# Kernel tuning notes

Measured on AMD Instinct MI355X. Metric: run time of the kernel, lower is better.

The kernel has to match this reference:

```python
import jax, jax.numpy as jnp
import numpy as np

N, E, F, S, R, H = 10000, 160000, 128, 10, 8, 64
SH_OFF = [0, 1, 4, 9]
SH_DIM = [1, 3, 5, 7]
AVG_NUM_NEIGHBORS = 16.0


def setup_inputs() -> dict:
    key = jax.random.key(0)
    ks = jax.random.split(key, 16)
    species = jax.random.randint(ks[0], (N,), 0, S)
    node_attrs = jax.nn.one_hot(species, S, dtype=jnp.float32)
    node_feats = jax.random.normal(ks[1], (N, F), dtype=jnp.float32)
    edge_attrs = jax.random.normal(ks[2], (E, 16), dtype=jnp.float32)
    edge_feats = jax.random.normal(ks[3], (E, R), dtype=jnp.float32)
    edge_index = jax.random.randint(ks[4], (2, E), 0, N)
    # learned parameters
    W_skip_node = jax.random.normal(ks[5], (F, S, F), dtype=jnp.float32)
    W_up = jax.random.normal(ks[6], (F, F), dtype=jnp.float32)
    mlp_w1 = jax.random.normal(ks[7], (R, H), dtype=jnp.float32)
    mlp_w2 = jax.random.normal(ks[8], (H, H), dtype=jnp.float32)
    mlp_w3 = jax.random.normal(ks[9], (H, H), dtype=jnp.float32)
    mlp_w4 = jax.random.normal(ks[10], (H, 4 * F), dtype=jnp.float32)  # conv_tp.weight_numel = 512
    W_lin = jax.random.normal(ks[11], (4, F, F), dtype=jnp.float32)
    W_skip_msg = jax.random.normal(ks[12], (4, F, S, F), dtype=jnp.float32)
    W_out = jax.random.normal(ks[13], (F, F), dtype=jnp.float32)
    return dict(node_attrs=node_attrs, node_feats=node_feats, edge_attrs=edge_attrs,
                edge_feats=edge_feats, edge_index=edge_index, species=species,
                W_skip_node=W_skip_node, W_up=W_up, mlp_w1=mlp_w1, mlp_w2=mlp_w2,
                mlp_w3=mlp_w3, mlp_w4=mlp_w4, W_lin=W_lin, W_skip_msg=W_skip_msg,
                W_out=W_out)


def reference(node_attrs, node_feats, edge_attrs, edge_feats, edge_index, species,
              W_skip_node, W_up, mlp_w1, mlp_w2, mlp_w3, mlp_w4,
              W_lin, W_skip_msg, W_out):
    sender, receiver = edge_index[0], edge_index[1]
    num_nodes = node_feats.shape[0]
    num_edges = edge_attrs.shape[0]

    # skip_tp_node: FullyConnectedTensorProduct(128x0e, 10x0e -> 128x0e), fan_in = 128*10
    skip = jnp.einsum('nu,nv,uvw->nw', node_feats, node_attrs, W_skip_node) * (1.0 / np.sqrt(F * S))

    # linear_up: 128x0e -> 128x0e
    h = (node_feats @ W_up) * (1.0 / np.sqrt(F))

    # radial MLP (e3nn FullyConnectedNet: no bias, w/sqrt(fan_in), silu on hidden layers)
    t = edge_feats
    for W in (mlp_w1, mlp_w2, mlp_w3):
        t = jax.nn.silu((t @ W) * (1.0 / np.sqrt(W.shape[0])))
    tp_w = (t @ mlp_w4) * (1.0 / np.sqrt(H))  # [E, 512]

    # conv_tp (gather -> 0e x l -> l 'uvu' TP) fused with scatter_sum per l-block
    hs = h[sender]  # [E, 128]
    msgs = []
    for l in range(4):
        d = SH_DIM[l]
        w_l = tp_w[:, l * F:(l + 1) * F]                       # [E, 128]
        sh_l = edge_attrs[:, SH_OFF[l]:SH_OFF[l] + d]          # [E, d]
        mji = (hs * w_l)[:, :, None] * sh_l[:, None, :]        # [E, 128, d]
        m = jax.ops.segment_sum(mji.reshape(num_edges, F * d), receiver,
                                num_segments=num_nodes)
        msgs.append(m.reshape(num_nodes, F, d))

    inv_avg = 1.0 / np.sqrt(AVG_NUM_NEIGHBORS)
    # linear (per-l 128->128) / sqrt(avg_num_neighbors), then skip_tp_msg (x 10x0e attrs)
    blocks = []
    for l in range(4):
        x = jnp.einsum('num,uw->nwm', msgs[l], W_lin[l]) * (inv_avg / np.sqrt(F))
        x = jnp.einsum('num,nv,uvw->nwm', x, node_attrs, W_skip_msg[l]) * (1.0 / np.sqrt(F * S))
        blocks.append(x)

    # linear_out: target -> 128x0e keeps only the scalar (l=0) block
    message = (blocks[0][:, :, 0] @ W_out) * (1.0 / np.sqrt(F))  # [N, 128]
    return message, skip
```

## Files before the change

### kernel.cpp

```cpp
#include <hip/hip_runtime.h>
#include <math.h>

#define NFEAT 128
#define NSPEC 10

__global__ void k_histboth(const int* __restrict__ species, const int* __restrict__ edge_index,
                           int* __restrict__ counts, int* __restrict__ ehist, int N, int E) {
    int i = blockIdx.x * blockDim.x + threadIdx.x;
    if (i < N) atomicAdd(&counts[species[i]], 1);
    if (i < E) atomicAdd(&ehist[edge_index[E + i]], 1);
}

__global__ void k_build(const int* __restrict__ counts, int* __restrict__ cursor,
                        int4* __restrict__ table, int* __restrict__ nTiles) {
    __shared__ int off[NSPEC + 1], ts[NSPEC + 1], cnt[NSPEC];
    const int t = threadIdx.x;
    if (t == 0) {
        int o = 0, tt = 0;
        for (int s = 0; s < NSPEC; s++) {
            cnt[s] = counts[s];
            off[s] = o; ts[s] = tt;
            o += cnt[s]; tt += (cnt[s] + 63) >> 6;
        }
        off[NSPEC] = o; ts[NSPEC] = tt;
        nTiles[0] = tt;
    }
    __syncthreads();
    if (t < NSPEC) cursor[t] = off[t];
    int nt = ts[NSPEC];
    for (int i = t; i < nt; i += blockDim.x) {
        int s = 0;
        while (ts[s + 1] <= i) s++;
        int b = i - ts[s];
        table[i] = make_int4(s, off[s] + b * 64, min(64, cnt[s] - b * 64), 0);
    }
}

__global__ void k_scatter(const int* __restrict__ species, int* __restrict__ cursor,
                          int* __restrict__ sorted, int N) {
    int i = blockIdx.x * blockDim.x + threadIdx.x;
    if (i < N) {
        int p = atomicAdd(&cursor[species[i]], 1);
        sorted[p] = i;
    }
}

__global__ void k_escan(const int* __restrict__ ehist, int* __restrict__ ecursor, int N) {
    __shared__ int ssum[256];
    const int t = threadIdx.x;
    const int chunk = (N + 255) / 256;
    const int lo = t * chunk;
    const int hi = min(lo + chunk, N);
    int local = 0;
    for (int i = lo; i < hi; i++) local += ehist[i];
    ssum[t] = local;
    __syncthreads();
    for (int off = 1; off < 256; off <<= 1) {
        int x = (t >= off) ? ssum[t - off] : 0;
        __syncthreads();
        ssum[t] += x;
        __syncthreads();
    }
    int run = ssum[t] - local;
    for (int i = lo; i < hi; i++) {
        ecursor[i] = run;
        run += ehist[i];
    }
}

__global__ void k_egather(const int* __restrict__ edge_index, const float* __restrict__ edge_attrs,
                          const float* __restrict__ edge_feats, int* __restrict__ ecursor,
                          int* __restrict__ sendG, int* __restrict__ recvG,
                          float* __restrict__ sh0G, float* __restrict__ efG, int E) {
    int i = blockIdx.x * blockDim.x + threadIdx.x;
    if (i < E) {
        int r = edge_index[E + i];
        int p = atomicAdd(&ecursor[r], 1);
        sendG[p] = edge_index[i];
        recvG[p] = r;
        sh0G[p]  = edge_attrs[(long)i * 16];
        float4 v0 = *(const float4*)(edge_feats + (long)i * 8);
        float4 v1 = *(const float4*)(edge_feats + (long)i * 8 + 4);
        *(float4*)(efG + (long)p * 8)     = v0;
        *(float4*)(efG + (long)p * 8 + 4) = v1;
    }
}

template <int BC>
__global__ __launch_bounds__(256) void k_gemm(
    const float* __restrict__ A, int aStride,
    const float* __restrict__ B, int bStride, int bSpecStride,
    float* __restrict__ C, int cStride, int cChunkY,
    int M, float alpha,
    const int* __restrict__ sorted,
    const int4* __restrict__ table,
    const int* __restrict__ nTiles)
{
    __shared__ float At[128][64];
    __shared__ float Bs[128][BC];
    const int t = threadIdx.x;
    const int gy = blockIdx.y;

    int start, cnt, spec = 0;
    if (table) {
        if (blockIdx.x >= nTiles[0]) return;
        int4 te = table[blockIdx.x];
        spec = te.x; start = te.y; cnt = te.z;
    } else {
        start = blockIdx.x * 64;
        cnt = M - start;
        if (cnt <= 0) return;
        if (cnt > 64) cnt = 64;
    }

    {
        const float* Bp = B + (long)spec * bSpecStride + (long)gy * BC;
        constexpr int F4R = BC / 4;
        #pragma unroll
        for (int i = 0; i < (128 * F4R) / 256; i++) {
            int idx = t + 256 * i;
            int k = idx / F4R;
            int c = (idx % F4R) * 4;
            *(float4*)&Bs[k][c] = *(const float4*)(Bp + (long)k * bStride + c);
        }
    }
    {
        int r = t & 63;
        int kc = (t >> 6) * 32;
        if (r < cnt) {
            int grow = table ? sorted[start + r] : (start + r);
            const float4* src = (const float4*)(A + (long)grow * aStride + kc);
            #pragma unroll
            for (int i = 0; i < 8; i++) {
                float4 v = src[i];
                At[kc + 4*i + 0][r] = v.x;
                At[kc + 4*i + 1][r] = v.y;
                At[kc + 4*i + 2][r] = v.z;
                At[kc + 4*i + 3][r] = v.w;
            }
        } else {
            #pragma unroll
            for (int i = 0; i < 32; i++) At[kc + i][r] = 0.0f;
        }
    }
    __syncthreads();

    constexpr int CG   = BC / 4;
    constexpr int ROWS = BC / 16;
    const int c0 = (t % CG) * 4;
    const int r0 = (t / CG) * ROWS;
    float acc[ROWS][4] = {};
    #pragma unroll 8
    for (int k = 0; k < 128; k++) {
        float4 b = *(const float4*)&Bs[k][c0];
        float av[ROWS];
        #pragma unroll
        for (int i = 0; i < ROWS / 4; i++) {
            float4 a = *(const float4*)&At[k][r0 + 4 * i];
            av[4*i + 0] = a.x; av[4*i + 1] = a.y; av[4*i + 2] = a.z; av[4*i + 3] = a.w;
        }
        #pragma unroll
        for (int i = 0; i < ROWS; i++) {
            acc[i][0] += av[i] * b.x;
            acc[i][1] += av[i] * b.y;
            acc[i][2] += av[i] * b.z;
            acc[i][3] += av[i] * b.w;
        }
    }
    #pragma unroll
    for (int i = 0; i < ROWS; i++) {
        int r = r0 + i;
        if (r < cnt) {
            int grow = table ? sorted[start + r] : (start + r);
            float4 v = make_float4(acc[i][0] * alpha, acc[i][1] * alpha,
                                   acc[i][2] * alpha, acc[i][3] * alpha);
            *(float4*)&C[(long)gy * cChunkY + (long)grow * cStride + c0] = v;
        }
    }
}

__global__ __launch_bounds__(256) void k_edge(
    const int*   __restrict__ sendG,
    const int*   __restrict__ recvG,
    const float* __restrict__ sh0G,
    const float* __restrict__ efG,
    const float* __restrict__ W1,
    const float* __restrict__ W2,
    const float* __restrict__ W3,
    const float* __restrict__ W4,
    const float* __restrict__ h,
    float*       __restrict__ msgs0,
    int E)
{
    __shared__ float W1s[8][64];
    __shared__ float W2s[64][64];
    __shared__ float act[64][64];
    __shared__ float efT[8][64];
    __shared__ int   sendS[64];
    __shared__ int   recvS[64];
    __shared__ float sh0S[64];

    const int t = threadIdx.x;
    if (t < 128) ((float4*)W1s)[t] = ((const float4*)W1)[t];
    #pragma unroll
    for (int i = 0; i < 4; i++)
        ((float4*)W2s)[t + 256 * i] = ((const float4*)W2)[t + 256 * i];
    __syncthreads();

    const float s1 = 0.3535533905932738f;
    const float s2 = 0.125f;

    const int e0 = (t & 15) * 4;
    const int j0 = (t >> 4) * 4;

    int ntiles = (E + 63) >> 6;
    for (int tile = blockIdx.x; tile < ntiles; tile += gridDim.x) {
        int ebase = tile << 6;
        if (t < 64) {
            int p = ebase + t;
            if (p < E) {
                sendS[t] = sendG[p];
                recvS[t] = recvG[p];
                sh0S[t]  = sh0G[p];
            } else { sendS[t] = 0; recvS[t] = -1; sh0S[t] = 0.0f; }
        } else if (t < 128) {
            int l = t - 64;
            int p = ebase + l;
            if (p < E) {
                float4 v0 = *(const float4*)(efG + (long)p * 8);
                float4 v1 = *(const float4*)(efG + (long)p * 8 + 4);
                efT[0][l] = v0.x; efT[1][l] = v0.y; efT[2][l] = v0.z; efT[3][l] = v0.w;
                efT[4][l] = v1.x; efT[5][l] = v1.y; efT[6][l] = v1.z; efT[7][l] = v1.w;
            } else {
                #pragma unroll
                for (int k = 0; k < 8; k++) efT[k][l] = 0.0f;
            }
        }
        __syncthreads();

        {
            float acc[4][4] = {};
            #pragma unroll
            for (int k = 0; k < 8; k++) {
                float4 a = *(const float4*)&efT[k][e0];
                float4 b = *(const float4*)&W1s[k][j0];
                float av[4] = {a.x, a.y, a.z, a.w};
                float bv[4] = {b.x, b.y, b.z, b.w};
                #pragma unroll
                for (int jj = 0; jj < 4; jj++)
                    #pragma unroll
                    for (int ee = 0; ee < 4; ee++)
                        acc[jj][ee] += av[ee] * bv[jj];
            }
            #pragma unroll
            for (int jj = 0; jj < 4; jj++) {
                float4 v; float x;
                x = acc[jj][0] * s1; v.x = x / (1.0f + __expf(-x));
                x = acc[jj][1] * s1; v.y = x / (1.0f + __expf(-x));
                x = acc[jj][2] * s1; v.z = x / (1.0f + __expf(-x));
                x = acc[jj][3] * s1; v.w = x / (1.0f + __expf(-x));
                *(float4*)&act[j0 + jj][e0] = v;
            }
        }
        __syncthreads();

        {
            float acc[4][4] = {};
            #pragma unroll 4
            for (int k = 0; k < 64; k++) {
                float4 a = *(const float4*)&act[k][e0];
                float4 b = *(const float4*)&W2s[k][j0];
                float av[4] = {a.x, a.y, a.z, a.w};
                float bv[4] = {b.x, b.y, b.z, b.w};
                #pragma unroll
                for (int jj = 0; jj < 4; jj++)
                    #pragma unroll
                    for (int ee = 0; ee < 4; ee++)
                        acc[jj][ee] += av[ee] * bv[jj];
            }
            __syncthreads();
            #pragma unroll
            for (int jj = 0; jj < 4; jj++) {
                float4 v; float x;
                x = acc[jj][0] * s2; v.x = x / (1.0f + __expf(-x));
                x = acc[jj][1] * s2; v.y = x / (1.0f + __expf(-x));
                x = acc[jj][2] * s2; v.z = x / (1.0f + __expf(-x));
                x = acc[jj][3] * s2; v.w = x / (1.0f + __expf(-x));
                *(float4*)&act[j0 + jj][e0] = v;
            }
        }
        __syncthreads();

        {
            float acc[4][4] = {};
            #pragma unroll 4
            for (int k = 0; k < 64; k++) {
                float4 a = *(const float4*)&act[k][e0];
                float4 b = *(const float4*)(W3 + k * 64 + j0);
                float av[4] = {a.x, a.y, a.z, a.w};
                float bv[4] = {b.x, b.y, b.z, b.w};
                #pragma unroll
                for (int jj = 0; jj < 4; jj++)
                    #pragma unroll
                    for (int ee = 0; ee < 4; ee++)
                        acc[jj][ee] += av[ee] * bv[jj];
            }
            __syncthreads();
            #pragma unroll
            for (int jj = 0; jj < 4; jj++) {
                float4 v; float x;
                x = acc[jj][0] * s2; v.x = x / (1.0f + __expf(-x));
                x = acc[jj][1] * s2; v.y = x / (1.0f + __expf(-x));
                x = acc[jj][2] * s2; v.z = x / (1.0f + __expf(-x));
                x = acc[jj][3] * s2; v.w = x / (1.0f + __expf(-x));
                *(float4*)&act[j0 + jj][e0] = v;
            }
        }
        __syncthreads();

        {
            const int c0  = (t & 31) * 4;
            const int ew0 = (t >> 5) * 8;
            float acc[8][4] = {};
            #pragma unroll 4
            for (int k = 0; k < 64; k++) {
                float4 b  = *(const float4*)&W4[k * 512 + c0];
                float4 a0 = *(const float4*)&act[k][ew0];
                float4 a1 = *(const float4*)&act[k][ew0 + 4];
                float av[8] = {a0.x, a0.y, a0.z, a0.w, a1.x, a1.y, a1.z, a1.w};
                #pragma unroll
                for (int i = 0; i < 8; i++) {
                    acc[i][0] += av[i] * b.x;
                    acc[i][1] += av[i] * b.y;
                    acc[i][2] += av[i] * b.z;
                    acc[i][3] += av[i] * b.w;
                }
            }
            float4 sum = make_float4(0.f, 0.f, 0.f, 0.f);
            int cur = recvS[ew0];
            #pragma unroll
            for (int i = 0; i < 8; i++) {
                int el = ew0 + i;
                int rcv = recvS[el];
                float f = sh0S[el] * s2;
                int snd = sendS[el];
                float4 hv = *(const float4*)&h[(long)snd * NFEAT + c0];
                float4 v = make_float4(acc[i][0] * f * hv.x, acc[i][1] * f * hv.y,
                                       acc[i][2] * f * hv.z, acc[i][3] * f * hv.w);
                if (rcv != cur) {
                    if (cur >= 0) {
                        float* dst = msgs0 + (long)cur * NFEAT + c0;
                        atomicAdd(dst + 0, sum.x); atomicAdd(dst + 1, sum.y);
                        atomicAdd(dst + 2, sum.z); atomicAdd(dst + 3, sum.w);
                    }
                    cur = rcv; sum = v;
                } else {
                    sum.x += v.x; sum.y += v.y; sum.z += v.z; sum.w += v.w;
                }
            }
            if (cur >= 0) {
                float* dst = msgs0 + (long)cur * NFEAT + c0;
                atomicAdd(dst + 0, sum.x); atomicAdd(dst + 1, sum.y);
                atomicAdd(dst + 2, sum.z); atomicAdd(dst + 3, sum.w);
            }
        }
        __syncthreads();
    }
}

extern "C" void kernel_launch(void* const* d_in, const int* in_sizes, int n_in,
                              void* d_out, int out_size, void* d_ws, size_t ws_size,
                              hipStream_t stream) {
    const float* node_feats = (const float*)d_in[1];
    const float* edge_attrs = (const float*)d_in[2];
    const float* edge_feats = (const float*)d_in[3];
    const int*   edge_index = (const int*)  d_in[4];
    const int*   species    = (const int*)  d_in[5];
    const float* Wsn        = (const float*)d_in[6];
    const float* Wup        = (const float*)d_in[7];
    const float* W1         = (const float*)d_in[8];
    const float* W2         = (const float*)d_in[9];
    const float* W3         = (const float*)d_in[10];
    const float* W4         = (const float*)d_in[11];
    const float* Wlin       = (const float*)d_in[12];
    const float* Wsm        = (const float*)d_in[13];
    const float* Wout       = (const float*)d_in[14];

    const int N = in_sizes[5];
    const int E = in_sizes[4] / 2;
    const int NF = NFEAT;

    float* out     = (float*)d_out;
    float* message = out;
    float* skip    = out + (long)N * NF;

    char* wsb = (char*)d_ws;
    size_t off = 0;
    auto carve = [&](size_t bytes) { void* p = wsb + off; off = (off + bytes + 255) & ~(size_t)255; return p; };
    float* h      = (float*)carve((size_t)N * NF * 4);
    float* msgs0  = (float*)carve((size_t)N * NF * 4);
    float* Tst    = (float*)carve((size_t)NSPEC * NF * NF * 4);
    float* Comb   = (float*)carve((size_t)NSPEC * NF * NF * 4);
    int*   sorted = (int*)carve((size_t)N * 4);
    int*   counts = (int*)carve(64);
    int*   cursor = (int*)carve(64);
    int*   nTiles = (int*)carve(16);
    int4*  table  = (int4*)carve(256 * 16);
    int*   ehist  = (int*)carve((size_t)N * 4);
    int*   ecursor= (int*)carve((size_t)N * 4);
    int*   sendG  = (int*)carve((size_t)E * 4);
    int*   recvG  = (int*)carve((size_t)E * 4);
    float* sh0G   = (float*)carve((size_t)E * 4);
    float* efG    = (float*)carve((size_t)E * 8 * 4);

    const float aH    = 1.0f / sqrtf((float)NF);
    const float aSkip = 1.0f / sqrtf((float)(NF * NSPEC));
    const float cTot  = 0.25f / ((float)NF * sqrtf((float)(NF * NSPEC)));

    hipMemsetAsync(counts, 0, 64, stream);
    hipMemsetAsync(ehist, 0, (size_t)N * 4, stream);
    hipMemsetAsync(msgs0, 0, (size_t)N * NF * 4, stream);

    k_histboth<<<(max(N, E) + 255) / 256, 256, 0, stream>>>(species, edge_index, counts, ehist, N, E);
    k_build  <<<1, 256, 0, stream>>>(counts, cursor, table, nTiles);
    k_scatter<<<(N + 255) / 256, 256, 0, stream>>>(species, cursor, sorted, N);
    k_escan  <<<1, 256, 0, stream>>>(ehist, ecursor, N);
    k_egather<<<(E + 255) / 256, 256, 0, stream>>>(edge_index, edge_attrs, edge_feats,
                                                   ecursor, sendG, recvG, sh0G, efG, E);

    const int mTiles   = (N + 63) / 64;
    const int maxTiles = mTiles + NSPEC;

    k_gemm<64><<<dim3(mTiles, 2), 256, 0, stream>>>(
        node_feats, NF, Wup, NF, 0, h, NF, 64, N, aH, nullptr, nullptr, nullptr);

    k_gemm<128><<<dim3(2, NSPEC), 256, 0, stream>>>(
        Wlin, NF, Wsm, NF * NSPEC, 0, Tst, NF, NF * NF, NF, 1.0f, nullptr, nullptr, nullptr);

    k_gemm<128><<<dim3((NSPEC * NF) / 64, 1), 256, 0, stream>>>(
        Tst, NF, Wout, NF, 0, Comb, NF, NF, NSPEC * NF, cTot, nullptr, nullptr, nullptr);

    k_gemm<64><<<dim3(maxTiles, 2), 256, 0, stream>>>(
        node_feats, NF, Wsn, NF * NSPEC, NF, skip, NF, 64, N, aSkip, sorted, table, nTiles);

    int edgeTiles = (E + 63) / 64;
    int edgeGrid  = edgeTiles < 1024 ? edgeTiles : 1024;
    k_edge<<<edgeGrid, 256, 0, stream>>>(
        sendG, recvG, sh0G, efG, W1, W2, W3, W4, h, msgs0, E);

    k_gemm<64><<<dim3(maxTiles, 2), 256, 0, stream>>>(
        msgs0, NF, Comb, NF, NF * NF, message, NF, 64, N, 1.0f, sorted, table, nTiles);
}
```

Baseline: 363.9 us.

## Restructure edge MLP to per-wavefront 16-edge tiles and fuse up/skip node GEMMs

The edge kernel now gives each 64-lane wavefront its own 16-edge tile with private LDS activations, so block-wide __syncthreads between MLP layers disappear. It uses a full grid instead of a persistent loop and reads W2/W3 directly from global/cache. A new k_hs kernel fuses the linear_up and species-sorted skip GEMMs so node feature tiles are loaded into LDS once. In exchange, each W4 row and each h gather is amortised over fewer edges, and more atomics may be issued per receiver because segments are split at finer granularity.

```diff
diff --git a/kernel.cpp b/kernel.cpp
--- a/kernel.cpp
+++ b/kernel.cpp
@@ -179,7 +179,90 @@
     }
 }
 
-__global__ __launch_bounds__(256) void k_edge(
+__global__ __launch_bounds__(256) void k_hs(
+    const float* __restrict__ A,
+    const float* __restrict__ Wup,
+    const float* __restrict__ Wsn,
+    float* __restrict__ h, float* __restrict__ skip,
+    const int* __restrict__ sorted, const int4* __restrict__ table,
+    const int* __restrict__ nTiles, float aH, float aSkip)
+{
+    __shared__ float At[128][64];
+    __shared__ float Bs[128][64];
+    const int t = threadIdx.x;
+    const int gy = blockIdx.y;
+    if (blockIdx.x >= nTiles[0]) return;
+    int4 te = table[blockIdx.x];
+    const int spec = te.x, start = te.y, cnt = te.z;
+
+    {
+        int r = t & 63, kc = (t >> 6) * 32;
+        if (r < cnt) {
+            int grow = sorted[start + r];
+            const float4* src = (const float4*)(A + (long)grow * NFEAT + kc);
+            #pragma unroll
+            for (int i = 0; i < 8; i++) {
+                float4 v = src[i];
+                At[kc + 4*i + 0][r] = v.x;
+                At[kc + 4*i + 1][r] = v.y;
+                At[kc + 4*i + 2][r] = v.z;
+                At[kc + 4*i + 3][r] = v.w;
+            }
+        } else {
+            #pragma unroll
+            for (int i = 0; i < 32; i++) At[kc + i][r] = 0.0f;
+        }
+    }
+    const int c0 = (t & 15) * 4;
+    const int r0 = (t >> 4) * 4;
+    #pragma unroll
+    for (int pass = 0; pass < 2; pass++) {
+        {
+            const float* Bp = pass == 0 ? (Wup + gy * 64)
+                                        : (Wsn + spec * NFEAT + gy * 64);
+            const int bStride = pass == 0 ? NFEAT : NFEAT * NSPEC;
+            #pragma unroll
+            for (int i = 0; i < 8; i++) {
+                int idx = t + 256 * i;
+                int k = idx >> 4;
+                int c = (idx & 15) * 4;
+                *(float4*)&Bs[k][c] = *(const float4*)(Bp + (long)k * bStride + c);
+            }
+        }
+        __syncthreads();
+        float acc[4][4] = {};
+        #pragma unroll 8
+        for (int k = 0; k < 128; k++) {
+            float4 b = *(const float4*)&Bs[k][c0];
+            float4 a = *(const float4*)&At[k][r0];
+            float av[4] = {a.x, a.y, a.z, a.w};
+            #pragma unroll
+            for (int i = 0; i < 4; i++) {
+                acc[i][0] += av[i] * b.x;
+                acc[i][1] += av[i] * b.y;
+                acc[i][2] += av[i] * b.z;
+                acc[i][3] += av[i] * b.w;
+            }
+        }
+        float* dst   = pass == 0 ? h : skip;
+        float  alpha = pass == 0 ? aH : aSkip;
+        #pragma unroll
+        for (int i = 0; i < 4; i++) {
+            int r = r0 + i;
+            if (r < cnt) {
+                int grow = sorted[start + r];
+                float4 v = make_float4(acc[i][0] * alpha, acc[i][1] * alpha,
+                                       acc[i][2] * alpha, acc[i][3] * alpha);
+                *(float4*)&dst[(long)grow * NFEAT + gy * 64 + c0] = v;
+            }
+        }
+        __syncthreads();
+    }
+}
+
+#define ASTR 20
+
+__global__ __launch_bounds__(256, 5) void k_edge(
     const int*   __restrict__ sendG,
     const int*   __restrict__ recvG,
     const float* __restrict__ sh0G,
@@ -193,178 +276,163 @@
     int E)
 {
     __shared__ float W1s[8][64];
-    __shared__ float W2s[64][64];
-    __shared__ float act[64][64];
-    __shared__ float efT[8][64];
-    __shared__ int   sendS[64];
-    __shared__ int   recvS[64];
-    __shared__ float sh0S[64];
+    __shared__ float actS[4][64 * ASTR];
+    __shared__ float efS[4][8 * 16];
+    __shared__ int   sendS[4][16];
+    __shared__ int   recvS[4][16];
+    __shared__ float sh0S[4][16];
 
     const int t = threadIdx.x;
     if (t < 128) ((float4*)W1s)[t] = ((const float4*)W1)[t];
-    #pragma unroll
-    for (int i = 0; i < 4; i++)
-        ((float4*)W2s)[t + 256 * i] = ((const float4*)W2)[t + 256 * i];
     __syncthreads();
+
+    const int wid = t >> 6, lane = t & 63;
+    const int ntiles = (E + 15) >> 4;
+    const int tile = blockIdx.x * 4 + wid;
+    if (tile >= ntiles) return;
+    const int base = tile << 4;
+
+    float* act = actS[wid];
+    float* ef  = efS[wid];
+
+    {
+        int g = lane & 15, p = base + g;
+        bool ok = p < E;
+        if (lane < 16)      sendS[wid][g] = ok ? sendG[p] : 0;
+        else if (lane < 32) recvS[wid][g] = ok ? recvG[p] : -1;
+        else if (lane < 48) sh0S[wid][g]  = ok ? sh0G[p]  : 0.0f;
+    }
+    {
+        int idx = lane * 2, e = idx >> 3, k = idx & 7;
+        int p = base + e;
+        float2 v = make_float2(0.f, 0.f);
+        if (p < E) v = *(const float2*)(efG + (long)p * 8 + k);
+        ef[k * 16 + e]       = v.x;
+        ef[(k + 1) * 16 + e] = v.y;
+    }
 
     const float s1 = 0.3535533905932738f;
     const float s2 = 0.125f;
-
-    const int e0 = (t & 15) * 4;
-    const int j0 = (t >> 4) * 4;
-
-    int ntiles = (E + 63) >> 6;
-    for (int tile = blockIdx.x; tile < ntiles; tile += gridDim.x) {
-        int ebase = tile << 6;
-        if (t < 64) {
-            int p = ebase + t;
-            if (p < E) {
-                sendS[t] = sendG[p];
-                recvS[t] = recvG[p];
-                sh0S[t]  = sh0G[p];
-            } else { sendS[t] = 0; recvS[t] = -1; sh0S[t] = 0.0f; }
-        } else if (t < 128) {
-            int l = t - 64;
-            int p = ebase + l;
-            if (p < E) {
-                float4 v0 = *(const float4*)(efG + (long)p * 8);
-                float4 v1 = *(const float4*)(efG + (long)p * 8 + 4);
-                efT[0][l] = v0.x; efT[1][l] = v0.y; efT[2][l] = v0.z; efT[3][l] = v0.w;
-                efT[4][l] = v1.x; efT[5][l] = v1.y; efT[6][l] = v1.z; efT[7][l] = v1.w;
-            } else {
+    const int e4 = lane & 3;
+    const int j4 = lane >> 2;
+
+    {
+        float acc[4][4] = {};
+        #pragma unroll
+        for (int k = 0; k < 8; k++) {
+            float4 a = *(const float4*)&ef[k * 16 + e4 * 4];
+            float4 b = *(const float4*)&W1s[k][j4 * 4];
+            float av[4] = {a.x, a.y, a.z, a.w};
+            float bv[4] = {b.x, b.y, b.z, b.w};
+            #pragma unroll
+            for (int jj = 0; jj < 4; jj++)
                 #pragma unroll
-                for (int k = 0; k < 8; k++) efT[k][l] = 0.0f;
-            }
-        }
-        __syncthreads();
-
-        {
-            float acc[4][4] = {};
-            #pragma unroll
-            for (int k = 0; k < 8; k++) {
-                float4 a = *(const float4*)&efT[k][e0];
-                float4 b = *(const float4*)&W1s[k][j0];
-                float av[4] = {a.x, a.y, a.z, a.w};
-                float bv[4] = {b.x, b.y, b.z, b.w};
+                for (int ee = 0; ee < 4; ee++)
+                    acc[jj][ee] += av[ee] * bv[jj];
+        }
+        #pragma unroll
+        for (int jj = 0; jj < 4; jj++) {
+            float4 v; float x;
+            x = acc[jj][0] * s1; v.x = x / (1.0f + __expf(-x));
+            x = acc[jj][1] * s1; v.y = x / (1.0f + __expf(-x));
+            x = acc[jj][2] * s1; v.z = x / (1.0f + __expf(-x));
+            x = acc[jj][3] * s1; v.w = x / (1.0f + __expf(-x));
+            *(float4*)&act[(j4 * 4 + jj) * ASTR + e4 * 4] = v;
+        }
+    }
+
+    {
+        float acc[4][4] = {};
+        const float4* W2v = (const float4*)W2;
+        #pragma unroll 4
+        for (int k = 0; k < 64; k++) {
+            float4 a = *(const float4*)&act[k * ASTR + e4 * 4];
+            float4 b = W2v[k * 16 + j4];
+            float av[4] = {a.x, a.y, a.z, a.w};
+            float bv[4] = {b.x, b.y, b.z, b.w};
+            #pragma unroll
+            for (int jj = 0; jj < 4; jj++)
                 #pragma unroll
-                for (int jj = 0; jj < 4; jj++)
-                    #pragma unroll
-                    for (int ee = 0; ee < 4; ee++)
-                        acc[jj][ee] += av[ee] * bv[jj];
-            }
-            #pragma unroll
-            for (int jj = 0; jj < 4; jj++) {
-                float4 v; float x;
-                x = acc[jj][0] * s1; v.x = x / (1.0f + __expf(-x));
-                x = acc[jj][1] * s1; v.y = x / (1.0f + __expf(-x));
-                x = acc[jj][2] * s1; v.z = x / (1.0f + __expf(-x));
-                x = acc[jj][3] * s1; v.w = x / (1.0f + __expf(-x));
-                *(float4*)&act[j0 + jj][e0] = v;
-            }
-        }
-        __syncthreads();
-
-        {
-            float acc[4][4] = {};
-            #pragma unroll 4
-            for (int k = 0; k < 64; k++) {
-                float4 a = *(const float4*)&act[k][e0];
-                float4 b = *(const float4*)&W2s[k][j0];
-                float av[4] = {a.x, a.y, a.z, a.w};
-                float bv[4] = {b.x, b.y, b.z, b.w};
+                for (int ee = 0; ee < 4; ee++)
+                    acc[jj][ee] += av[ee] * bv[jj];
+        }
+        #pragma unroll
+        for (int jj = 0; jj < 4; jj++) {
+            float4 v; float x;
+            x = acc[jj][0] * s2; v.x = x / (1.0f + __expf(-x));
+            x = acc[jj][1] * s2; v.y = x / (1.0f + __expf(-x));
+            x = acc[jj][2] * s2; v.z = x / (1.0f + __expf(-x));
+            x = acc[jj][3] * s2; v.w = x / (1.0f + __expf(-x));
+            *(float4*)&act[(j4 * 4 + jj) * ASTR + e4 * 4] = v;
+        }
+    }
+
+    {
+        float acc[4][4] = {};
+        const float4* W3v = (const float4*)W3;
+        #pragma unroll 4
+        for (int k = 0; k < 64; k++) {
+            float4 a = *(const float4*)&act[k * ASTR + e4 * 4];
+            float4 b = W3v[k * 16 + j4];
+            float av[4] = {a.x, a.y, a.z, a.w};
+            float bv[4] = {b.x, b.y, b.z, b.w};
+            #pragma unroll
+            for (int jj = 0; jj < 4; jj++)
                 #pragma unroll
-                for (int jj = 0; jj < 4; jj++)
-                    #pragma unroll
-                    for (int ee = 0; ee < 4; ee++)
-                        acc[jj][ee] += av[ee] * bv[jj];
-            }
-            __syncthreads();
-            #pragma unroll
-            for (int jj = 0; jj < 4; jj++) {
-                float4 v; float x;
-                x = acc[jj][0] * s2; v.x = x / (1.0f + __expf(-x));
-                x = acc[jj][1] * s2; v.y = x / (1.0f + __expf(-x));
-                x = acc[jj][2] * s2; v.z = x / (1.0f + __expf(-x));
-                x = acc[jj][3] * s2; v.w = x / (1.0f + __expf(-x));
-                *(float4*)&act[j0 + jj][e0] = v;
-            }
-        }
-        __syncthreads();
-
-        {
-            float acc[4][4] = {};
-            #pragma unroll 4
-            for (int k = 0; k < 64; k++) {
-                float4 a = *(const float4*)&act[k][e0];
-                float4 b = *(const float4*)(W3 + k * 64 + j0);
-                float av[4] = {a.x, a.y, a.z, a.w};
-                float bv[4] = {b.x, b.y, b.z, b.w};
-                #pragma unroll
-                for (int jj = 0; jj < 4; jj++)
-                    #pragma unroll
-                    for (int ee = 0; ee < 4; ee++)
-                        acc[jj][ee] += av[ee] * bv[jj];
-            }
-            __syncthreads();
-            #pragma unroll
-            for (int jj = 0; jj < 4; jj++) {
-                float4 v; float x;
-                x = acc[jj][0] * s2; v.x = x / (1.0f + __expf(-x));
-                x = acc[jj][1] * s2; v.y = x / (1.0f + __expf(-x));
-                x = acc[jj][2] * s2; v.z = x / (1.0f + __expf(-x));
-                x = acc[jj][3] * s2; v.w = x / (1.0f + __expf(-x));
-                *(float4*)&act[j0 + jj][e0] = v;
-            }
-        }
-        __syncthreads();
-
-        {
-            const int c0  = (t & 31) * 4;
-            const int ew0 = (t >> 5) * 8;
-            float acc[8][4] = {};
-            #pragma unroll 4
-            for (int k = 0; k < 64; k++) {
-                float4 b  = *(const float4*)&W4[k * 512 + c0];
-                float4 a0 = *(const float4*)&act[k][ew0];
-                float4 a1 = *(const float4*)&act[k][ew0 + 4];
-                float av[8] = {a0.x, a0.y, a0.z, a0.w, a1.x, a1.y, a1.z, a1.w};
-                #pragma unroll
-                for (int i = 0; i < 8; i++) {
-                    acc[i][0] += av[i] * b.x;
-                    acc[i][1] += av[i] * b.y;
-                    acc[i][2] += av[i] * b.z;
-                    acc[i][3] += av[i] * b.w;
+                for (int ee = 0; ee < 4; ee++)
+                    acc[jj][ee] += av[ee] * bv[jj];
+        }
+        #pragma unroll
+        for (int jj = 0; jj < 4; jj++) {
+            float4 v; float x;
+            x = acc[jj][0] * s2; v.x = x / (1.0f + __expf(-x));
+            x = acc[jj][1] * s2; v.y = x / (1.0f + __expf(-x));
+            x = acc[jj][2] * s2; v.z = x / (1.0f + __expf(-x));
+            x = acc[jj][3] * s2; v.w = x / (1.0f + __expf(-x));
+            *(float4*)&act[(j4 * 4 + jj) * ASTR + e4 * 4] = v;
+        }
+    }
+
+    {
+        const int c0 = lane * 2;
+        float wacc[16][2] = {};
+        #pragma unroll 4
+        for (int k = 0; k < 64; k++) {
+            float2 w4 = *(const float2*)&W4[k * 512 + c0];
+            float4 a0 = *(const float4*)&act[k * ASTR + 0];
+            float4 a1 = *(const float4*)&act[k * ASTR + 4];
+            float4 a2 = *(const float4*)&act[k * ASTR + 8];
+            float4 a3 = *(const float4*)&act[k * ASTR + 12];
+            float av[16] = {a0.x, a0.y, a0.z, a0.w, a1.x, a1.y, a1.z, a1.w,
+                            a2.x, a2.y, a2.z, a2.w, a3.x, a3.y, a3.z, a3.w};
+            #pragma unroll
+            for (int e = 0; e < 16; e++) {
+                wacc[e][0] += av[e] * w4.x;
+                wacc[e][1] += av[e] * w4.y;
+            }
+        }
+        int cur = recvS[wid][0];
+        float sum0 = 0.f, sum1 = 0.f;
+        #pragma unroll
+        for (int e = 0; e < 16; e++) {
+            int rcv = recvS[wid][e];
+            if (rcv != cur) {
+                if (cur >= 0) {
+                    atomicAdd(&msgs0[(long)cur * NFEAT + c0],     sum0);
+                    atomicAdd(&msgs0[(long)cur * NFEAT + c0 + 1], sum1);
                 }
-            }
-            float4 sum = make_float4(0.f, 0.f, 0.f, 0.f);
-            int cur = recvS[ew0];
-            #pragma unroll
-            for (int i = 0; i < 8; i++) {
-                int el = ew0 + i;
-                int rcv = recvS[el];
-                float f = sh0S[el] * s2;
-                int snd = sendS[el];
-                float4 hv = *(const float4*)&h[(long)snd * NFEAT + c0];
-                float4 v = make_float4(acc[i][0] * f * hv.x, acc[i][1] * f * hv.y,
-                                       acc[i][2] * f * hv.z, acc[i][3] * f * hv.w);
-                if (rcv != cur) {
-                    if (cur >= 0) {
-                        float* dst = msgs0 + (long)cur * NFEAT + c0;
-                        atomicAdd(dst + 0, sum.x); atomicAdd(dst + 1, sum.y);
-                        atomicAdd(dst + 2, sum.z); atomicAdd(dst + 3, sum.w);
-                    }
-                    cur = rcv; sum = v;
-                } else {
-                    sum.x += v.x; sum.y += v.y; sum.z += v.z; sum.w += v.w;
-                }
-            }
-            if (cur >= 0) {
-                float* dst = msgs0 + (long)cur * NFEAT + c0;
-                atomicAdd(dst + 0, sum.x); atomicAdd(dst + 1, sum.y);
-                atomicAdd(dst + 2, sum.z); atomicAdd(dst + 3, sum.w);
-            }
-        }
-        __syncthreads();
+                cur = rcv; sum0 = 0.f; sum1 = 0.f;
+            }
+            float f = sh0S[wid][e] * s2;
+            int snd = sendS[wid][e];
+            float2 hv = *(const float2*)&h[(long)snd * NFEAT + c0];
+            sum0 += wacc[e][0] * f * hv.x;
+            sum1 += wacc[e][1] * f * hv.y;
+        }
+        if (cur >= 0) {
+            atomicAdd(&msgs0[(long)cur * NFEAT + c0],     sum0);
+            atomicAdd(&msgs0[(long)cur * NFEAT + c0 + 1], sum1);
+        }
     }
 }
 
@@ -431,8 +499,8 @@
     const int mTiles   = (N + 63) / 64;
     const int maxTiles = mTiles + NSPEC;
 
-    k_gemm<64><<<dim3(mTiles, 2), 256, 0, stream>>>(
-        node_feats, NF, Wup, NF, 0, h, NF, 64, N, aH, nullptr, nullptr, nullptr);
+    k_hs<<<dim3(maxTiles, 2), 256, 0, stream>>>(
+        node_feats, Wup, Wsn, h, skip, sorted, table, nTiles, aH, aSkip);
 
     k_gemm<128><<<dim3(2, NSPEC), 256, 0, stream>>>(
         Wlin, NF, Wsm, NF * NSPEC, 0, Tst, NF, NF * NF, NF, 1.0f, nullptr, nullptr, nullptr);
@@ -440,12 +508,9 @@
     k_gemm<128><<<dim3((NSPEC * NF) / 64, 1), 256, 0, stream>>>(
         Tst, NF, Wout, NF, 0, Comb, NF, NF, NSPEC * NF, cTot, nullptr, nullptr, nullptr);
 
-    k_gemm<64><<<dim3(maxTiles, 2), 256, 0, stream>>>(
-        node_feats, NF, Wsn, NF * NSPEC, NF, skip, NF, 64, N, aSkip, sorted, table, nTiles);
-
-    int edgeTiles = (E + 63) / 64;
-    int edgeGrid  = edgeTiles < 1024 ? edgeTiles : 1024;
-    k_edge<<<edgeGrid, 256, 0, stream>>>(
+    int eTiles = (E + 15) / 16;
+    int eBlocks = (eTiles + 3) / 4;
+    k_edge<<<eBlocks, 256, 0, stream>>>(
         sendG, recvG, sh0G, efG, W1, W2, W3, W4, h, msgs0, E);
 
     k_gemm<64><<<dim3(maxTiles, 2), 256, 0, stream>>>(
```

Result: no change. 362.9 us (-0.3%).
